# Kernel optimization log

Measured on AMD Instinct MI355X. Metric: run time of the kernel, lower is better.

Reference implementation:

```python
import jax, jax.numpy as jnp
import numpy as np

H = 32          # voxel bins per axis (init kwarg)
NB = H + 1      # floor((x-min)/((max-min)/H)) can hit H at the max point
EPS = 1e-5


def setup_inputs() -> dict:
    key = jax.random.key(0)
    ks = jax.random.split(key, 7)
    B, N = 4, 32768
    pt_cloud = jax.random.normal(ks[0], (B, N, 3), dtype=jnp.float32)
    def conv_params(k, cin, cout):
        k1, k2 = jax.random.split(k)
        s = 1.0 / np.sqrt(cin)
        W = jax.random.uniform(k1, (cout, cin), jnp.float32, -s, s)
        b = jax.random.uniform(k2, (cout,), jnp.float32, -s, s)
        return W, b
    W1, b1 = conv_params(ks[1], 4, 64)
    W2, b2 = conv_params(ks[2], 64, 128)
    W3, b3 = conv_params(ks[3], 128, 1024)
    return {
        "pt_cloud": pt_cloud,
        "W1": W1, "b1": b1, "g1": jnp.ones(64), "beta1": jnp.zeros(64),
        "W2": W2, "b2": b2, "g2": jnp.ones(128), "beta2": jnp.zeros(128),
        "W3": W3, "b3": b3, "g3": jnp.ones(1024), "beta3": jnp.zeros(1024),
    }


def _embed(pt_cloud):
    # Voxel-quantize points using global (over whole batch) per-axis min/max,
    # then attach the occupancy count of each point's voxel -> [B, N, 4].
    B, N, _ = pt_cloud.shape
    mins = pt_cloud.min(axis=(0, 1))           # [3]
    maxs = pt_cloud.max(axis=(0, 1))           # [3]
    v = jnp.floor((pt_cloud - mins) / ((maxs - mins) / H))  # [B,N,3] voxel coords
    vi = v.astype(jnp.int32)
    ids = (vi[..., 0] * NB + vi[..., 1]) * NB + vi[..., 2]  # [B,N] voxel id
    flat = (jnp.arange(B, dtype=jnp.int32)[:, None] * (NB ** 3) + ids).reshape(-1)
    # histogram: count points per (batch, voxel) bin, then gather back per point
    counts = jax.ops.segment_sum(jnp.ones_like(flat, jnp.float32), flat,
                                 num_segments=B * NB ** 3)
    cnt = counts[flat].reshape(B, N, 1)
    return jnp.concatenate([v, cnt], axis=-1)  # [B,N,4]


def _bn(x, g, b):
    # training-mode BatchNorm1d over (B, N) per channel (biased variance)
    m = x.mean(axis=(0, 1))
    var = x.var(axis=(0, 1))
    return g * (x - m) * jax.lax.rsqrt(var + EPS) + b


def _block(x, W, b, g, beta):
    # conv1x1 == pointwise matmul: [B,N,Cin] x [Cout,Cin] -> [B,N,Cout]
    y = jnp.einsum('bnc,oc->bno', x, W) + b
    return jax.nn.relu(_bn(y, g, beta))


def reference(pt_cloud, W1, b1, g1, beta1, W2, b2, g2, beta2, W3, b3, g3, beta3):
    x = _embed(pt_cloud)
    x = _block(x, W1, b1, g1, beta1)
    x = _block(x, W2, b2, g2, beta2)
    x = _block(x, W3, b3, g3, beta3)
    return x  # [B, N, 1024]
```

## Files before the change

### kernel.cpp

```cpp
#include <hip/hip_runtime.h>

#define HB 32
#define NBv 33
#define NB3 35937
#define BN_EPS 1e-5f

using short8 = __attribute__((ext_vector_type(8))) short;
using f32x4  = __attribute__((ext_vector_type(4))) float;
using US = unsigned short;

__device__ __forceinline__ unsigned fenc(float f){ unsigned u=__float_as_uint(f); return (u&0x80000000u)? ~u : (u|0x80000000u); }
__device__ __forceinline__ float fdec(unsigned e){ return (e&0x80000000u)? __uint_as_float(e&0x7fffffffu) : __uint_as_float(~e); }
__device__ __forceinline__ US f2bf(float f){ unsigned u=__float_as_uint(f); return (US)((u + 0x7fffu + ((u>>16)&1u))>>16); }
__device__ __forceinline__ float bf2f(US b){ return __uint_as_float(((unsigned)b)<<16); }

__global__ __launch_bounds__(256) void k_init(unsigned* __restrict__ mm, unsigned* __restrict__ counts,
    float* __restrict__ stat0, float* __restrict__ sum1, float* __restrict__ S1,
    float* __restrict__ sum2, float* __restrict__ S2) {
  int i = blockIdx.x*256 + threadIdx.x;
  if (i<6) mm[i] = (i<3)? 0xFFFFFFFFu : 0u;
  if (i<NB3*4) counts[i]=0u;
  if (i<14) stat0[i]=0.f;
  if (i<64) sum1[i]=0.f;
  if (i<4096) S1[i]=0.f;
  if (i<128) sum2[i]=0.f;
  if (i<16384) S2[i]=0.f;
}

__global__ __launch_bounds__(256) void k_minmax(const float* __restrict__ pc, unsigned* __restrict__ mm, int npts) {
  int tid = threadIdx.x;
  int gid = blockIdx.x*256+tid, stride = gridDim.x*256;
  float mn0=3.4e38f,mn1=3.4e38f,mn2=3.4e38f, mx0=-3.4e38f,mx1=-3.4e38f,mx2=-3.4e38f;
  for (int p=gid;p<npts;p+=stride){
    float a=pc[3*p], b=pc[3*p+1], c=pc[3*p+2];
    mn0=fminf(mn0,a); mx0=fmaxf(mx0,a);
    mn1=fminf(mn1,b); mx1=fmaxf(mx1,b);
    mn2=fminf(mn2,c); mx2=fmaxf(mx2,c);
  }
  __shared__ float red[256];
  float v[6] = {mn0,mn1,mn2,mx0,mx1,mx2};
  #pragma unroll
  for (int q=0;q<6;q++){
    red[tid]=v[q]; __syncthreads();
    for (int st=128;st;st>>=1){ if (tid<st) red[tid] = (q<3)? fminf(red[tid],red[tid+st]) : fmaxf(red[tid],red[tid+st]); __syncthreads(); }
    if (tid==0){ if (q<3) atomicMin(&mm[q], fenc(red[0])); else atomicMax(&mm[q], fenc(red[0])); }
    __syncthreads();
  }
}

__device__ __forceinline__ void get_mm(const unsigned* __restrict__ mm, float* mins, float* step){
  #pragma unroll
  for (int a=0;a<3;a++){ float mn=fdec(mm[a]), mx=fdec(mm[3+a]); mins[a]=mn; step[a]=(mx-mn)*(1.0f/HB); }
}
__device__ __forceinline__ int vox(const float* __restrict__ pc, int p, const float* mins, const float* step, float* v){
  float v0 = floorf((pc[3*p+0]-mins[0])/step[0]);
  float v1 = floorf((pc[3*p+1]-mins[1])/step[1]);
  float v2 = floorf((pc[3*p+2]-mins[2])/step[2]);
  v[0]=v0; v[1]=v1; v[2]=v2;
  return ((int)v0*NBv + (int)v1)*NBv + (int)v2;
}

__global__ __launch_bounds__(256) void k_hist(const float* __restrict__ pc, const unsigned* __restrict__ mm,
    unsigned* __restrict__ counts, int npts, int perB) {
  int p = blockIdx.x*256+threadIdx.x; if (p>=npts) return;
  float mins[3], step[3]; get_mm(mm,mins,step);
  float v[3]; int id = vox(pc,p,mins,step,v);
  atomicAdd(&counts[(p/perB)*NB3 + id], 1u);
}

__global__ __launch_bounds__(256) void k_embedstats(const float* __restrict__ pc, const unsigned* __restrict__ mm,
    const unsigned* __restrict__ counts, float* __restrict__ stat0, int npts, int perB) {
  int tid=threadIdx.x; int gid=blockIdx.x*256+tid, stride=gridDim.x*256;
  float mins[3], step[3]; get_mm(mm,mins,step);
  float s0=0,s1=0,s2=0,s3=0;
  float P[10]={0,0,0,0,0,0,0,0,0,0};
  for (int p=gid;p<npts;p+=stride){
    float v[3]; int id=vox(pc,p,mins,step,v);
    float x0=v[0],x1=v[1],x2=v[2],x3=(float)counts[(p/perB)*NB3+id];
    s0+=x0; s1+=x1; s2+=x2; s3+=x3;
    P[0]+=x0*x0; P[1]+=x0*x1; P[2]+=x0*x2; P[3]+=x0*x3;
    P[4]+=x1*x1; P[5]+=x1*x2; P[6]+=x1*x3;
    P[7]+=x2*x2; P[8]+=x2*x3; P[9]+=x3*x3;
  }
  __shared__ float red[256];
  float vals[14]={s0,s1,s2,s3,P[0],P[1],P[2],P[3],P[4],P[5],P[6],P[7],P[8],P[9]};
  #pragma unroll
  for (int q=0;q<14;q++){
    red[tid]=vals[q]; __syncthreads();
    for (int st=128;st;st>>=1){ if(tid<st) red[tid]+=red[tid+st]; __syncthreads(); }
    if (!tid) atomicAdd(&stat0[q], red[0]);
    __syncthreads();
  }
}

__global__ __launch_bounds__(64) void k_stats1(const float* __restrict__ stat0, const float* __restrict__ W1,
    const float* __restrict__ b1, const float* __restrict__ g1, const float* __restrict__ be1,
    float* __restrict__ A1, float* __restrict__ c1, int npts) {
  int o = threadIdx.x;
  float inv = 1.0f/(float)npts;
  float mu0=stat0[0]*inv, mu1=stat0[1]*inv, mu2=stat0[2]*inv, mu3=stat0[3]*inv;
  float w0=W1[o*4],w1=W1[o*4+1],w2=W1[o*4+2],w3=W1[o*4+3];
  float wmu = w0*mu0+w1*mu1+w2*mu2+w3*mu3;
  const float* T = stat0+4;
  float q = w0*w0*T[0] + 2.f*w0*w1*T[1] + 2.f*w0*w2*T[2] + 2.f*w0*w3*T[3]
          + w1*w1*T[4] + 2.f*w1*w2*T[5] + 2.f*w1*w3*T[6]
          + w2*w2*T[7] + 2.f*w2*w3*T[8] + w3*w3*T[9];
  float var = q*inv - wmu*wmu;
  float s = g1[o]*rsqrtf(var+BN_EPS);
  A1[o*4]=s*w0; A1[o*4+1]=s*w1; A1[o*4+2]=s*w2; A1[o*4+3]=s*w3;
  c1[o] = be1[o] - s*wmu;
}

__global__ __launch_bounds__(256) void k_layer1(const float* __restrict__ pc, const unsigned* __restrict__ mm,
    const unsigned* __restrict__ counts, const float* __restrict__ A1, const float* __restrict__ c1,
    US* __restrict__ x1, int npts, int perB) {
  __shared__ float sA[256]; __shared__ float sc[64];
  int tid=threadIdx.x;
  sA[tid]=A1[tid]; if (tid<64) sc[tid]=c1[tid];
  __syncthreads();
  int p = blockIdx.x*256+tid; if (p>=npts) return;
  float mins[3], step[3]; get_mm(mm,mins,step);
  float v[3]; int id=vox(pc,p,mins,step,v);
  float cnt=(float)counts[(p/perB)*NB3+id];
  float a0=v[0],a1=v[1],a2=v[2],a3=cnt;
  __align__(16) US ob[64];
  #pragma unroll
  for (int o=0;o<64;o++){
    float y = sc[o] + sA[o*4]*a0 + sA[o*4+1]*a1 + sA[o*4+2]*a2 + sA[o*4+3]*a3;
    ob[o]=f2bf(fmaxf(y,0.f));
  }
  uint4* dst=(uint4*)&x1[(size_t)p*64];
  const uint4* sb=(const uint4*)ob;
  #pragma unroll
  for (int i=0;i<8;i++) dst[i]=sb[i];
}

template<int C>
__global__ __launch_bounds__(256) void k_transpose(const US* __restrict__ X, US* __restrict__ XT,
    float* __restrict__ sums, int M) {
  __shared__ US tile[64][74];
  constexpr int TC = C/64;
  int bt = blockIdx.x;
  int pb = (bt/TC)*64, cb = (bt%TC)*64;
  int t = threadIdx.x;
  #pragma unroll
  for (int i=0;i<4;i++){
    int idx = t*4 + i*1024; int p = idx>>6, c = idx&63;
    const US* src = &X[(size_t)(pb+p)*C + cb + c];
    ushort2 v0 = *(const ushort2*)src; ushort2 v1 = *(const ushort2*)(src+2);
    tile[p][c]=v0.x; tile[p][c+1]=v0.y; tile[p][c+2]=v1.x; tile[p][c+3]=v1.y;
  }
  __syncthreads();
  int cc = t>>2, g = t&3;
  float s = 0.f;
  __align__(16) US buf[16];
  #pragma unroll
  for (int q=0;q<16;q++){ buf[q]=tile[g*16+q][cc]; s += bf2f(buf[q]); }
  US* dst = &XT[(size_t)(cb+cc)*M + pb + g*16];
  ((uint4*)dst)[0]=((const uint4*)buf)[0];
  ((uint4*)dst)[1]=((const uint4*)buf)[1];
  s += __shfl_down(s,1); s += __shfl_down(s,2);
  if (g==0) atomicAdd(&sums[cb+cc], s);
}

template<int C, int IT>
__global__ __launch_bounds__(256) void k_cov(const US* __restrict__ XT, float* __restrict__ S, int M, int kpb) {
  constexpr int JT = C/16;
  int w = threadIdx.x>>6, lane = threadIdx.x&63;
  int r = lane&15, h = lane>>4;
  int k0 = blockIdx.x*kpb;
  f32x4 acc[IT][JT];
  #pragma unroll
  for (int it=0;it<IT;it++)
    #pragma unroll
    for (int jt=0;jt<JT;jt++) acc[it][jt]=f32x4{0.f,0.f,0.f,0.f};
  for (int kk=0; kk<kpb; kk+=32){
    int kb = k0 + kk + h*8;
    short8 a[IT], b[JT];
    #pragma unroll
    for (int it=0;it<IT;it++) a[it] = *(const short8*)&XT[(size_t)((w+it*4)*16 + r)*M + kb];
    #pragma unroll
    for (int jt=0;jt<JT;jt++) b[jt] = *(const short8*)&XT[(size_t)(jt*16 + r)*M + kb];
    #pragma unroll
    for (int it=0;it<IT;it++)
      #pragma unroll
      for (int jt=0;jt<JT;jt++)
        acc[it][jt] = __builtin_amdgcn_mfma_f32_16x16x32_bf16(a[it], b[jt], acc[it][jt], 0,0,0);
  }
  #pragma unroll
  for (int it=0;it<IT;it++)
    #pragma unroll
    for (int jt=0;jt<JT;jt++)
      #pragma unroll
      for (int j=0;j<4;j++)
        atomicAdd(&S[((w+it*4)*16 + h*4 + j)*C + jt*16 + r], acc[it][jt][j]);
}

__global__ __launch_bounds__(64) void k_stats2(const float* __restrict__ sum1, const float* __restrict__ S1,
    const float* __restrict__ W2, const float* __restrict__ b2, const float* __restrict__ g2, const float* __restrict__ be2,
    US* __restrict__ A2, float* __restrict__ c2, int npts) {
  int o = blockIdx.x, t = threadIdx.x;
  __shared__ float sw[64];
  sw[t] = W2[o*64+t];
  __syncthreads();
  float inv = 1.0f/(float)npts;
  float wi = sw[t];
  float d=0.f;
  #pragma unroll 8
  for (int j=0;j<64;j++) d += S1[t*64+j]*sw[j];
  float part = wi*d;
  float wmup = wi*sum1[t]*inv;
  #pragma unroll
  for (int off=32;off;off>>=1){ part+=__shfl_down(part,off); wmup+=__shfl_down(wmup,off); }
  float q = __shfl(part,0), wmu = __shfl(wmup,0);
  float var = q*inv - wmu*wmu;
  float s = g2[o]*rsqrtf(var+BN_EPS);
  A2[o*64+t] = f2bf(s*sw[t]);
  if (t==0) c2[o] = be2[o] - s*wmu;
}

__global__ __launch_bounds__(128) void k_stats3(const float* __restrict__ sum2, const float* __restrict__ S2,
    const float* __restrict__ W3, const float* __restrict__ b3, const float* __restrict__ g3, const float* __restrict__ be3,
    US* __restrict__ A3, float* __restrict__ c3, int npts) {
  int o = blockIdx.x, t = threadIdx.x;
  __shared__ float sw[128], red[128], red2[128];
  sw[t] = W3[o*128+t];
  __syncthreads();
  float inv = 1.0f/(float)npts;
  float wi = sw[t];
  float d=0.f;
  #pragma unroll 8
  for (int j=0;j<128;j++) d += S2[t*128+j]*sw[j];
  red[t] = wi*d; red2[t] = wi*sum2[t]*inv;
  __syncthreads();
  for (int st=64; st; st>>=1){ if (t<st){ red[t]+=red[t+st]; red2[t]+=red2[t+st]; } __syncthreads(); }
  float q = red[0], wmu = red2[0];
  float var = q*inv - wmu*wmu;
  float s = g3[o]*rsqrtf(var+BN_EPS);
  A3[o*128+t] = f2bf(s*sw[t]);
  if (t==0) c3[o] = be3[o] - s*wmu;
}

template<int K, int NT, int NOUT, bool OUTBF16>
__global__ __launch_bounds__(256) void k_gemm(const US* __restrict__ X, const US* __restrict__ Wf,
    const float* __restrict__ cvec, void* __restrict__ outp, int M) {
  constexpr int G = NOUT/(16*NT);
  int wid = (blockIdx.x*256 + threadIdx.x)>>6;
  int lane = threadIdx.x&63;
  int ptTile = wid / G, cg = wid % G;
  int ptbase = ptTile*16, obase = cg*16*NT;
  int r = lane&15, h = lane>>4;
  f32x4 acc[NT];
  #pragma unroll
  for (int t=0;t<NT;t++) acc[t]=f32x4{0.f,0.f,0.f,0.f};
  const US* arow = X + (size_t)(ptbase + r)*K + h*8;
  #pragma unroll
  for (int k=0;k<K;k+=32){
    short8 a = *(const short8*)(arow + k);
    #pragma unroll
    for (int t=0;t<NT;t++){
      short8 b = *(const short8*)(Wf + (size_t)(obase + t*16 + r)*K + k + h*8);
      acc[t] = __builtin_amdgcn_mfma_f32_16x16x32_bf16(a, b, acc[t], 0,0,0);
    }
  }
  #pragma unroll
  for (int t=0;t<NT;t++){
    int col = obase + t*16 + r;
    float ct = cvec[col];
    #pragma unroll
    for (int j=0;j<4;j++){
      int row = ptbase + h*4 + j;
      float vv = fmaxf(acc[t][j]+ct, 0.f);
      if (OUTBF16) ((US*)outp)[(size_t)row*NOUT+col] = f2bf(vv);
      else        ((float*)outp)[(size_t)row*NOUT+col] = vv;
    }
  }
}

extern "C" void kernel_launch(void* const* d_in, const int* in_sizes, int n_in,
                              void* d_out, int out_size, void* d_ws, size_t ws_size,
                              hipStream_t stream) {
  const float* pc  = (const float*)d_in[0];
  const float* W1  = (const float*)d_in[1];  const float* b1 = (const float*)d_in[2];
  const float* g1  = (const float*)d_in[3];  const float* be1= (const float*)d_in[4];
  const float* W2  = (const float*)d_in[5];  const float* b2 = (const float*)d_in[6];
  const float* g2  = (const float*)d_in[7];  const float* be2= (const float*)d_in[8];
  const float* W3  = (const float*)d_in[9];  const float* b3 = (const float*)d_in[10];
  const float* g3  = (const float*)d_in[11]; const float* be3= (const float*)d_in[12];
  int npts = in_sizes[0]/3;
  int perB = npts/4;

  char* ws = (char*)d_ws;
  size_t off = 0;
  auto alloc = [&](size_t bytes){ size_t o = off; off = (off + bytes + 255) & ~(size_t)255; return o; };
  unsigned* mm     = (unsigned*)(ws + alloc(6*4));
  unsigned* counts = (unsigned*)(ws + alloc((size_t)4*NB3*4));
  float* stat0 = (float*)(ws + alloc(14*4));
  float* A1    = (float*)(ws + alloc(256*4));
  float* c1    = (float*)(ws + alloc(64*4));
  float* sum1  = (float*)(ws + alloc(64*4));
  float* S1    = (float*)(ws + alloc(4096*4));
  US*    A2    = (US*)(ws + alloc(8192*2));
  float* c2    = (float*)(ws + alloc(128*4));
  float* sum2  = (float*)(ws + alloc(128*4));
  float* S2    = (float*)(ws + alloc(16384*4));
  US*    A3    = (US*)(ws + alloc(131072*2));
  float* c3    = (float*)(ws + alloc(1024*4));
  US* x1  = (US*)(ws + alloc((size_t)npts*64*2));
  US* x1T = (US*)(ws + alloc((size_t)npts*64*2));
  US* x2  = (US*)(ws + alloc((size_t)npts*128*2));
  US* x2T = (US*)(ws + alloc((size_t)npts*128*2));

  int pblk = (npts+255)/256;

  k_init<<<(NB3*4+255)/256,256,0,stream>>>(mm,counts,stat0,sum1,S1,sum2,S2);
  k_minmax<<<256,256,0,stream>>>(pc,mm,npts);
  k_hist<<<pblk,256,0,stream>>>(pc,mm,counts,npts,perB);
  k_embedstats<<<256,256,0,stream>>>(pc,mm,counts,stat0,npts,perB);
  k_stats1<<<1,64,0,stream>>>(stat0,W1,b1,g1,be1,A1,c1,npts);
  k_layer1<<<pblk,256,0,stream>>>(pc,mm,counts,A1,c1,x1,npts,perB);
  k_transpose<64><<<npts/64,256,0,stream>>>(x1,x1T,sum1,npts);
  k_cov<64,1><<<32,256,0,stream>>>(x1T,S1,npts,npts/32);
  k_stats2<<<128,64,0,stream>>>(sum1,S1,W2,b2,g2,be2,A2,c2,npts);
  k_gemm<64,4,128,true><<<(npts/16)*2/4,256,0,stream>>>(x1,A2,c2,x2,npts);
  k_transpose<128><<<(npts/64)*2,256,0,stream>>>(x2,x2T,sum2,npts);
  k_cov<128,2><<<32,256,0,stream>>>(x2T,S2,npts,npts/32);
  k_stats3<<<1024,128,0,stream>>>(sum2,S2,W3,b3,g3,be3,A3,c3,npts);
  k_gemm<128,8,1024,false><<<(npts/16)*8/4,256,0,stream>>>(x2,A3,c3,(float*)d_out,npts);
}
```

Measured before the change: 1.223 ms.

## Split covariance into per-block partials and use LDS-tiled GEMM for layers

```diff
diff --git a/kernel.cpp b/kernel.cpp
--- a/kernel.cpp
+++ b/kernel.cpp
@@ -9,22 +9,23 @@
 using f32x4  = __attribute__((ext_vector_type(4))) float;
 using US = unsigned short;
 
+#define GL_LDS16(gp, lp) __builtin_amdgcn_global_load_lds( \
+    (const __attribute__((address_space(1))) unsigned int*)(gp), \
+    (__attribute__((address_space(3))) unsigned int*)(lp), 16, 0, 0)
+
 __device__ __forceinline__ unsigned fenc(float f){ unsigned u=__float_as_uint(f); return (u&0x80000000u)? ~u : (u|0x80000000u); }
 __device__ __forceinline__ float fdec(unsigned e){ return (e&0x80000000u)? __uint_as_float(e&0x7fffffffu) : __uint_as_float(~e); }
 __device__ __forceinline__ US f2bf(float f){ unsigned u=__float_as_uint(f); return (US)((u + 0x7fffu + ((u>>16)&1u))>>16); }
 __device__ __forceinline__ float bf2f(US b){ return __uint_as_float(((unsigned)b)<<16); }
 
 __global__ __launch_bounds__(256) void k_init(unsigned* __restrict__ mm, unsigned* __restrict__ counts,
-    float* __restrict__ stat0, float* __restrict__ sum1, float* __restrict__ S1,
-    float* __restrict__ sum2, float* __restrict__ S2) {
+    float* __restrict__ stat0, float* __restrict__ sum1, float* __restrict__ sum2) {
   int i = blockIdx.x*256 + threadIdx.x;
   if (i<6) mm[i] = (i<3)? 0xFFFFFFFFu : 0u;
   if (i<NB3*4) counts[i]=0u;
   if (i<14) stat0[i]=0.f;
   if (i<64) sum1[i]=0.f;
-  if (i<4096) S1[i]=0.f;
   if (i<128) sum2[i]=0.f;
-  if (i<16384) S2[i]=0.f;
 }
 
 __global__ __launch_bounds__(256) void k_minmax(const float* __restrict__ pc, unsigned* __restrict__ mm, int npts) {
@@ -163,37 +164,38 @@
   if (g==0) atomicAdd(&sums[cb+cc], s);
 }
 
-template<int C, int IT>
-__global__ __launch_bounds__(256) void k_cov(const US* __restrict__ XT, float* __restrict__ S, int M, int kpb) {
+template<int C, int NW>
+__global__ __launch_bounds__(NW*64) void k_cov(const US* __restrict__ XT, float* __restrict__ P, int M, int kpb) {
   constexpr int JT = C/16;
   int w = threadIdx.x>>6, lane = threadIdx.x&63;
   int r = lane&15, h = lane>>4;
   int k0 = blockIdx.x*kpb;
-  f32x4 acc[IT][JT];
-  #pragma unroll
-  for (int it=0;it<IT;it++)
-    #pragma unroll
-    for (int jt=0;jt<JT;jt++) acc[it][jt]=f32x4{0.f,0.f,0.f,0.f};
+  f32x4 acc[JT];
+  #pragma unroll
+  for (int jt=0;jt<JT;jt++) acc[jt]=f32x4{0.f,0.f,0.f,0.f};
   for (int kk=0; kk<kpb; kk+=32){
     int kb = k0 + kk + h*8;
-    short8 a[IT], b[JT];
-    #pragma unroll
-    for (int it=0;it<IT;it++) a[it] = *(const short8*)&XT[(size_t)((w+it*4)*16 + r)*M + kb];
-    #pragma unroll
-    for (int jt=0;jt<JT;jt++) b[jt] = *(const short8*)&XT[(size_t)(jt*16 + r)*M + kb];
-    #pragma unroll
-    for (int it=0;it<IT;it++)
-      #pragma unroll
-      for (int jt=0;jt<JT;jt++)
-        acc[it][jt] = __builtin_amdgcn_mfma_f32_16x16x32_bf16(a[it], b[jt], acc[it][jt], 0,0,0);
-  }
-  #pragma unroll
-  for (int it=0;it<IT;it++)
-    #pragma unroll
-    for (int jt=0;jt<JT;jt++)
-      #pragma unroll
-      for (int j=0;j<4;j++)
-        atomicAdd(&S[((w+it*4)*16 + h*4 + j)*C + jt*16 + r], acc[it][jt][j]);
+    short8 a = *(const short8*)&XT[(size_t)(w*16 + r)*M + kb];
+    #pragma unroll
+    for (int jt=0;jt<JT;jt++){
+      short8 b = *(const short8*)&XT[(size_t)(jt*16 + r)*M + kb];
+      acc[jt] = __builtin_amdgcn_mfma_f32_16x16x32_bf16(a, b, acc[jt], 0,0,0);
+    }
+  }
+  float* Pb = P + (size_t)blockIdx.x*C*C;
+  #pragma unroll
+  for (int jt=0;jt<JT;jt++)
+    #pragma unroll
+    for (int j=0;j<4;j++)
+      Pb[(w*16 + h*4 + j)*C + jt*16 + r] = acc[jt][j];
+}
+
+template<int C>
+__global__ __launch_bounds__(256) void k_covred(const float* __restrict__ P, float* __restrict__ S, int nblk) {
+  int i = blockIdx.x*256 + threadIdx.x;
+  float s = 0.f;
+  for (int b=0;b<nblk;b++) s += P[(size_t)b*C*C + i];
+  S[i] = s;
 }
 
 __global__ __launch_bounds__(64) void k_stats2(const float* __restrict__ sum1, const float* __restrict__ S1,
@@ -207,7 +209,7 @@
   float wi = sw[t];
   float d=0.f;
   #pragma unroll 8
-  for (int j=0;j<64;j++) d += S1[t*64+j]*sw[j];
+  for (int j=0;j<64;j++) d += S1[j*64+t]*sw[j];
   float part = wi*d;
   float wmup = wi*sum1[t]*inv;
   #pragma unroll
@@ -230,7 +232,7 @@
   float wi = sw[t];
   float d=0.f;
   #pragma unroll 8
-  for (int j=0;j<128;j++) d += S2[t*128+j]*sw[j];
+  for (int j=0;j<128;j++) d += S2[j*128+t]*sw[j];
   red[t] = wi*d; red2[t] = wi*sum2[t]*inv;
   __syncthreads();
   for (int st=64; st; st>>=1){ if (t<st){ red[t]+=red[t+st]; red2[t]+=red2[t+st]; } __syncthreads(); }
@@ -241,38 +243,65 @@
   if (t==0) c3[o] = be3[o] - s*wmu;
 }
 
-template<int K, int NT, int NOUT, bool OUTBF16>
-__global__ __launch_bounds__(256) void k_gemm(const US* __restrict__ X, const US* __restrict__ Wf,
+template<int K, int OUTW, bool OUTBF16>
+__global__ __launch_bounds__(256) void k_tgemm(const US* __restrict__ X, const US* __restrict__ Wf,
     const float* __restrict__ cvec, void* __restrict__ outp, int M) {
-  constexpr int G = NOUT/(16*NT);
-  int wid = (blockIdx.x*256 + threadIdx.x)>>6;
-  int lane = threadIdx.x&63;
-  int ptTile = wid / G, cg = wid % G;
-  int ptbase = ptTile*16, obase = cg*16*NT;
-  int r = lane&15, h = lane>>4;
-  f32x4 acc[NT];
-  #pragma unroll
-  for (int t=0;t<NT;t++) acc[t]=f32x4{0.f,0.f,0.f,0.f};
-  const US* arow = X + (size_t)(ptbase + r)*K + h*8;
-  #pragma unroll
-  for (int k=0;k<K;k+=32){
-    short8 a = *(const short8*)(arow + k);
-    #pragma unroll
-    for (int t=0;t<NT;t++){
-      short8 b = *(const short8*)(Wf + (size_t)(obase + t*16 + r)*K + k + h*8);
-      acc[t] = __builtin_amdgcn_mfma_f32_16x16x32_bf16(a, b, acc[t], 0,0,0);
+  constexpr int NG  = OUTW/128;
+  constexpr int RS  = K*2;
+  constexpr int CHM = K/8 - 1;
+  constexpr int NQ  = (128*K*2)/4096;
+  __shared__ US lds[2*128*K];
+  US* ldsA = lds; US* ldsB = lds + 128*K;
+  int tid = threadIdx.x, l = tid&63, w = tid>>6;
+  int og = blockIdx.x % NG, mb = blockIdx.x / NG;
+  const US* Asrc = X  + (size_t)mb*128*K;
+  const US* Bsrc = Wf + (size_t)og*128*K;
+  #pragma unroll
+  for (int q=0;q<NQ;q++){
+    unsigned B = ((unsigned)(q*4+w)<<10) + ((unsigned)l<<4);
+    unsigned r = B / RS;
+    unsigned cs = ((B>>4)&CHM) ^ (r & CHM);
+    GL_LDS16(Asrc + r*K + cs*8, ldsA + (q*4+w)*512);
+    GL_LDS16(Bsrc + r*K + cs*8, ldsB + (q*4+w)*512);
+  }
+  __syncthreads();
+  int rbw = (w>>1)*64, cbw = (w&1)*64;
+  int r16 = l&15, hq = l>>4;
+  f32x4 acc[4][4];
+  #pragma unroll
+  for (int i=0;i<4;i++)
+    #pragma unroll
+    for (int j=0;j<4;j++) acc[i][j]=f32x4{0.f,0.f,0.f,0.f};
+  #pragma unroll
+  for (int ks=0; ks<K/32; ks++){
+    short8 af[4], bf[4];
+    int ca = ks*4 + hq;
+    #pragma unroll
+    for (int f=0; f<4; f++){
+      int Ra = rbw + f*16 + r16;
+      af[f] = *(const short8*)&ldsA[Ra*K + ((ca ^ (Ra&CHM))<<3)];
+      int Rb = cbw + f*16 + r16;
+      bf[f] = *(const short8*)&ldsB[Rb*K + ((ca ^ (Rb&CHM))<<3)];
     }
-  }
-  #pragma unroll
-  for (int t=0;t<NT;t++){
-    int col = obase + t*16 + r;
-    float ct = cvec[col];
-    #pragma unroll
-    for (int j=0;j<4;j++){
-      int row = ptbase + h*4 + j;
-      float vv = fmaxf(acc[t][j]+ct, 0.f);
-      if (OUTBF16) ((US*)outp)[(size_t)row*NOUT+col] = f2bf(vv);
-      else        ((float*)outp)[(size_t)row*NOUT+col] = vv;
+    #pragma unroll
+    for (int fi=0;fi<4;fi++)
+      #pragma unroll
+      for (int fj=0;fj<4;fj++)
+        acc[fi][fj] = __builtin_amdgcn_mfma_f32_16x16x32_bf16(af[fi], bf[fj], acc[fi][fj], 0,0,0);
+  }
+  #pragma unroll
+  for (int fj=0;fj<4;fj++){
+    int col = og*128 + cbw + fj*16 + r16;
+    float cv = cvec[col];
+    #pragma unroll
+    for (int fi=0;fi<4;fi++){
+      #pragma unroll
+      for (int j=0;j<4;j++){
+        int row = mb*128 + rbw + fi*16 + hq*4 + j;
+        float v = fmaxf(acc[fi][fj][j]+cv, 0.f);
+        if (OUTBF16) ((US*)outp)[(size_t)row*OUTW+col] = f2bf(v);
+        else        ((float*)outp)[(size_t)row*OUTW+col] = v;
+      }
     }
   }
 }
@@ -289,6 +318,7 @@
   const float* g3  = (const float*)d_in[11]; const float* be3= (const float*)d_in[12];
   int npts = in_sizes[0]/3;
   int perB = npts/4;
+  const int NCOV = 256;
 
   char* ws = (char*)d_ws;
   size_t off = 0;
@@ -306,6 +336,8 @@
   float* S2    = (float*)(ws + alloc(16384*4));
   US*    A3    = (US*)(ws + alloc(131072*2));
   float* c3    = (float*)(ws + alloc(1024*4));
+  float* P1    = (float*)(ws + alloc((size_t)NCOV*4096*4));
+  float* P2    = (float*)(ws + alloc((size_t)NCOV*16384*4));
   US* x1  = (US*)(ws + alloc((size_t)npts*64*2));
   US* x1T = (US*)(ws + alloc((size_t)npts*64*2));
   US* x2  = (US*)(ws + alloc((size_t)npts*128*2));
@@ -313,18 +345,20 @@
 
   int pblk = (npts+255)/256;
 
-  k_init<<<(NB3*4+255)/256,256,0,stream>>>(mm,counts,stat0,sum1,S1,sum2,S2);
+  k_init<<<(NB3*4+255)/256,256,0,stream>>>(mm,counts,stat0,sum1,sum2);
   k_minmax<<<256,256,0,stream>>>(pc,mm,npts);
   k_hist<<<pblk,256,0,stream>>>(pc,mm,counts,npts,perB);
   k_embedstats<<<256,256,0,stream>>>(pc,mm,counts,stat0,npts,perB);
   k_stats1<<<1,64,0,stream>>>(stat0,W1,b1,g1,be1,A1,c1,npts);
   k_layer1<<<pblk,256,0,stream>>>(pc,mm,counts,A1,c1,x1,npts,perB);
   k_transpose<64><<<npts/64,256,0,stream>>>(x1,x1T,sum1,npts);
-  k_cov<64,1><<<32,256,0,stream>>>(x1T,S1,npts,npts/32);
+  k_cov<64,4><<<NCOV,256,0,stream>>>(x1T,P1,npts,npts/NCOV);
+  k_covred<64><<<16,256,0,stream>>>(P1,S1,NCOV);
   k_stats2<<<128,64,0,stream>>>(sum1,S1,W2,b2,g2,be2,A2,c2,npts);
-  k_gemm<64,4,128,true><<<(npts/16)*2/4,256,0,stream>>>(x1,A2,c2,x2,npts);
+  k_tgemm<64,128,true><<<npts/128,256,0,stream>>>(x1,A2,c2,x2,npts);
   k_transpose<128><<<(npts/64)*2,256,0,stream>>>(x2,x2T,sum2,npts);
-  k_cov<128,2><<<32,256,0,stream>>>(x2T,S2,npts,npts/32);
+  k_cov<128,8><<<NCOV,512,0,stream>>>(x2T,P2,npts,npts/NCOV);
+  k_covred<128><<<64,256,0,stream>>>(P2,S2,NCOV);
   k_stats3<<<1024,128,0,stream>>>(sum2,S2,W3,b3,g3,be3,A3,c3,npts);
-  k_gemm<128,8,1024,false><<<(npts/16)*8/4,256,0,stream>>>(x2,A3,c3,(float*)d_out,npts);
-}
+  k_tgemm<128,1024,false><<<(npts/128)*8,256,0,stream>>>(x2,A3,c3,(float*)d_out,npts);
+}
```

Result: faster. 1.012 ms (-17.2%).
